# Optimization experiments

Measured on AMD Instinct MI355X. Metric: run time of the kernel, lower is better.

## Reference

```python
import jax, jax.numpy as jnp
import numpy as np

INPUT_SIZE = 16
K = 50
HIDDEN_COUNT = 25
FINAL_WIDTH = INPUT_SIZE + HIDDEN_COUNT * K  # 1266


def setup_inputs() -> dict:
    key = jax.random.key(0)
    k1, k2, k3, k4, k5 = jax.random.split(key, 5)
    B = 32768
    state = jax.random.normal(k1, (B, INPUT_SIZE), dtype=jnp.float32)
    # Zero-padded weight stack: layer i uses Ws[i, :, : INPUT_SIZE + i*K]
    Ws = jax.random.normal(k2, (HIDDEN_COUNT, K, FINAL_WIDTH), dtype=jnp.float32) * 0.05
    bs = jax.random.normal(k3, (HIDDEN_COUNT, K), dtype=jnp.float32) * 0.05
    Wout = jax.random.normal(k4, (FINAL_WIDTH, 1), dtype=jnp.float32) * 0.05
    bout = jax.random.normal(k5, (1,), dtype=jnp.float32) * 0.05
    return {"state": state, "Ws": Ws, "bs": bs, "Wout": Wout, "bout": bout}


def reference(state, Ws, bs, Wout, bout):
    x = state  # [B, 16], grows by 50 per layer
    for i in range(HIDDEN_COUNT):  # fixed-size structural loop over layers
        width = INPUT_SIZE + i * K
        w = Ws[i, :, :width]                       # [50, width] (static slice)
        y = jax.nn.leaky_relu(x @ w.T + bs[i], negative_slope=0.01)  # [B, 50]
        x = jnp.concatenate([x, y], axis=1)        # [B, width+50]
    return x @ Wout + bout  # [B, 1]
```

## Files before the change

kernel.cpp:

```cpp
#include <hip/hip_runtime.h>


#define IN 16
#define KJ 50
#define NL 25
#define FW 1266
#define TR 24
#define NB 1366
#define BTOT 32768
#define XSTR 1288
#define NTHREADS 512
#define XLO_OFF 61824
#define SLAB_OFF 123648
#define WOUT_OFF 148224
#define BIAS_OFF 153344
#define LDS_BYTES 158464
#define CHUNK_STRIDE 3200
#define TOTAL_CHUNKS 973

typedef __attribute__((ext_vector_type(8))) short bf16x8;
typedef __attribute__((ext_vector_type(16))) float f32x16;

__device__ __forceinline__ unsigned short bf16_hi(float x, float* hif) {
    unsigned u = __float_as_uint(x);
    unsigned h = (u + 0x8000u) >> 16;
    *hif = __uint_as_float(h << 16);
    return (unsigned short)h;
}
__device__ __forceinline__ unsigned short bf16_rnd(float x) {
    return (unsigned short)((__float_as_uint(x) + 0x8000u) >> 16);
}

__device__ __forceinline__ void split8(const float* __restrict__ rowp, int kb, int width,
                                       unsigned hi[4], unsigned lo[4]) {
#pragma unroll
    for (int p = 0; p < 4; ++p) {
        unsigned h2[2], l2[2];
#pragma unroll
        for (int q = 0; q < 2; ++q) {
            int k = kb + p * 2 + q;
            float v = (k < width) ? rowp[k] : 0.f;
            float hif;
            unsigned short h = bf16_hi(v, &hif);
            h2[q] = h;
            l2[q] = bf16_rnd(v - hif);
        }
        hi[p] = h2[0] | (h2[1] << 16);
        lo[p] = l2[0] | (l2[1] << 16);
    }
}

__global__ __launch_bounds__(64, 1) void split_w(const float* __restrict__ Ws,
                                                 char* __restrict__ wsbuf) {
    int rem = blockIdx.x, layer = 0;
    size_t off = 0;
    for (;;) {
        int c = (IN + KJ * layer + 15) >> 4;
        if (rem < c) break;
        rem -= c; off += (size_t)c * CHUNK_STRIDE; ++layer;
    }
    const int ci = rem, k0 = ci << 4, width = IN + KJ * layer;
    const float* Wl = Ws + (size_t)layer * KJ * FW;
    char* base = wsbuf + off + (size_t)ci * CHUNK_STRIDE;
    const int l = threadIdx.x, ll = l & 31, kh = l >> 5;
    const int kb = k0 + kh * 8;

    unsigned hi[4], lo[4];
    split8(Wl + (size_t)ll * FW, kb, width, hi, lo);
    *reinterpret_cast<uint4*>(base + l * 16)        = make_uint4(hi[0], hi[1], hi[2], hi[3]);
    *reinterpret_cast<uint4*>(base + 1024 + l * 16) = make_uint4(lo[0], lo[1], lo[2], lo[3]);
    if (ll < 18) {
        split8(Wl + (size_t)(32 + ll) * FW, kb, width, hi, lo);
        *reinterpret_cast<uint4*>(base + 2048 + (kh * 18 + ll) * 16) = make_uint4(hi[0], hi[1], hi[2], hi[3]);
        *reinterpret_cast<uint4*>(base + 2624 + (kh * 18 + ll) * 16) = make_uint4(lo[0], lo[1], lo[2], lo[3]);
    }
}

__device__ __forceinline__ void loadB2(const char* __restrict__ wb, int ci, int chunks,
                                       int n, int l, int ll, int kh,
                                       bf16x8& bh, bf16x8& bl) {
    bf16x8 z = {0, 0, 0, 0, 0, 0, 0, 0};
    bh = z; bl = z;
    if (ci < chunks) {
        const char* cb = wb + (size_t)ci * CHUNK_STRIDE;
        if (n == 0) {
            bh = *(const bf16x8*)(cb + l * 16);
            bl = *(const bf16x8*)(cb + 1024 + l * 16);
        } else if (ll < 18) {
            bh = *(const bf16x8*)(cb + (kh * 18 + ll) * 16);
            bl = *(const bf16x8*)(cb + 576 + (kh * 18 + ll) * 16);
        }
    }
}
__device__ __forceinline__ void loadG2(const char* __restrict__ wb, int c0, int chunks,
                                       int n, int l, int ll, int kh,
                                       bf16x8& b0h, bf16x8& b0l, bf16x8& b1h, bf16x8& b1l) {
    loadB2(wb, c0,     chunks, n, l, ll, kh, b0h, b0l);
    loadB2(wb, c0 + 4, chunks, n, l, ll, kh, b1h, b1l);
}

__device__ __forceinline__ void mfma3(const unsigned short* xrh, const unsigned short* xrl,
                                      int kof, const bf16x8 bh, const bf16x8 bl, f32x16& acc) {
    bf16x8 ah = *(const bf16x8*)(xrh + kof);
    bf16x8 al = *(const bf16x8*)(xrl + kof);
    acc = __builtin_amdgcn_mfma_f32_32x32x16_bf16(al, bh, acc, 0, 0, 0);
    acc = __builtin_amdgcn_mfma_f32_32x32x16_bf16(ah, bl, acc, 0, 0, 0);
    acc = __builtin_amdgcn_mfma_f32_32x32x16_bf16(ah, bh, acc, 0, 0, 0);
}

__global__ __launch_bounds__(NTHREADS, 2) void densenet_mfma(
    const float* __restrict__ state, const char* __restrict__ wsbuf,
    const float* __restrict__ bs,    const float* __restrict__ Wout,
    const float* __restrict__ bout,  float* __restrict__ out)
{
    __shared__ __align__(16) char lds[LDS_BYTES];
    unsigned short* xhi = (unsigned short*)lds;
    unsigned short* xlo = (unsigned short*)(lds + XLO_OFF);
    float* slab  = (float*)(lds + SLAB_OFF);
    float* woutl = (float*)(lds + WOUT_OFF);
    float* biasl = (float*)(lds + BIAS_OFF);

    const int tid = threadIdx.x;
    const int w   = tid >> 6;
    const int l   = tid & 63;
    const int ll  = l & 31, kh = l >> 5;
    const int kq  = w & 3;
    const int n   = w >> 2;
    const long row0 = (long)blockIdx.x * TR;

    {
        unsigned* p = (unsigned*)lds;
        for (int i = tid; i < (XLO_OFF * 2) / 4; i += NTHREADS) p[i] = 0u;
    }
    for (int i = tid; i < FW; i += NTHREADS)      woutl[i] = Wout[i];
    for (int i = tid; i < NL * KJ; i += NTHREADS) biasl[i] = bs[i];
    __syncthreads();
    if (tid < TR * IN) {
        int r = tid >> 4, c = tid & 15;
        if (row0 + r < BTOT) {
            float v = state[(row0 + r) * IN + c];
            float hif;
            xhi[r * XSTR + c] = bf16_hi(v, &hif);
            xlo[r * XSTR + c] = bf16_rnd(v - hif);
        }
    }
    __syncthreads();

    const unsigned short* xrh = xhi + ll * XSTR + (kh << 3);
    const unsigned short* xrl = xlo + ll * XSTR + (kh << 3);

    int width = IN;
    size_t wofs = 0;
    for (int layer = 0; layer < NL; ++layer) {
        const int chunks = (width + 15) >> 4;
        const char* wb = wsbuf + wofs + (n ? 2048 : 0);

        f32x16 a0, a1, a2, a3;
#pragma unroll
        for (int i = 0; i < 16; ++i) { a0[i] = 0.f; a1[i] = 0.f; a2[i] = 0.f; a3[i] = 0.f; }

        const int T  = (chunks > kq) ? ((chunks - kq + 3) >> 2) : 0;
        int NG = (T + 1) >> 1;
        NG += (NG & 1);

        if (NG > 0) {
            bf16x8 A0h, A0l, A1h, A1l, B0h, B0l, B1h, B1l;
            loadG2(wb, kq, chunks, n, l, ll, kh, A0h, A0l, A1h, A1l);
            for (int G = 0; G < NG; G += 2) {
                const int c0 = kq + (G << 3);
                loadG2(wb, c0 + 8, chunks, n, l, ll, kh, B0h, B0l, B1h, B1l);
                mfma3(xrh, xrl, (c0)     << 4, A0h, A0l, a0);
                mfma3(xrh, xrl, (c0 + 4) << 4, A1h, A1l, a1);
                if (G + 2 < NG)
                    loadG2(wb, c0 + 16, chunks, n, l, ll, kh, A0h, A0l, A1h, A1l);
                mfma3(xrh, xrl, (c0 + 8)  << 4, B0h, B0l, a2);
                mfma3(xrh, xrl, (c0 + 12) << 4, B1h, B1l, a3);
            }
        }

        {
            float* sl = slab + kq * 1536;
#pragma unroll
            for (int r = 0; r < 12; ++r) {
                float v = (a0[r] + a1[r]) + (a2[r] + a3[r]);
                int crow = (r & 3) + 8 * (r >> 2) + 4 * kh;
                sl[crow * 64 + n * 32 + ll] = v;
            }
        }
        __syncthreads();

#pragma unroll
        for (int it = 0; it < 3; ++it) {
            int idx = it * NTHREADS + tid;
            int row = idx >> 6, j = idx & 63;
            float s = (slab[row * 64 + j] + slab[1536 + row * 64 + j])
                    + (slab[3072 + row * 64 + j] + slab[4608 + row * 64 + j]);
            if (j < KJ) {
                s += biasl[layer * KJ + j];
                s = (s > 0.f) ? s : 0.01f * s;
                float hif;
                xhi[row * XSTR + width + j] = bf16_hi(s, &hif);
                xlo[row * XSTR + width + j] = bf16_rnd(s - hif);
            }
        }
        __syncthreads();

        width += KJ;
        wofs += (size_t)chunks * CHUNK_STRIDE;
    }

    const float b0 = bout[0];
#pragma unroll
    for (int rr = 0; rr < 3; ++rr) {
        const int row = w * 3 + rr;
        const long grow = row0 + row;
        const unsigned short* xh = xhi + row * XSTR;
        const unsigned short* xl = xlo + row * XSTR;
        float s = 0.f;
#pragma unroll
        for (int it = 0; it < 19; ++it) {
            int k = l + (it << 6);
            float xv = __uint_as_float((unsigned)xh[k] << 16)
                     + __uint_as_float((unsigned)xl[k] << 16);
            s += xv * woutl[k];
        }
        {
            int k = 1216 + l;
            if (k < FW) {
                float xv = __uint_as_float((unsigned)xh[k] << 16)
                         + __uint_as_float((unsigned)xl[k] << 16);
                s += xv * woutl[k];
            }
        }
#pragma unroll
        for (int m = 32; m >= 1; m >>= 1) s += __shfl_xor(s, m, 64);
        if (l == 0 && grow < BTOT) out[grow] = s + b0;
    }
}

extern "C" void kernel_launch(void* const* d_in, const int* in_sizes, int n_in,
                              void* d_out, int out_size, void* d_ws, size_t ws_size,
                              hipStream_t stream) {
    const float* state = (const float*)d_in[0];
    const float* Ws    = (const float*)d_in[1];
    const float* bs    = (const float*)d_in[2];
    const float* Wout  = (const float*)d_in[3];
    const float* bout  = (const float*)d_in[4];
    float* out = (float*)d_out;
    char* wsbuf = (char*)d_ws;

    split_w<<<dim3(TOTAL_CHUNKS), dim3(64), 0, stream>>>(Ws, wsbuf);
    densenet_mfma<<<dim3(NB), dim3(NTHREADS), 0, stream>>>(state, wsbuf, bs, Wout, bout, out);
}
```

Measured before the change: 512.3 us.

## Double block to 1024 threads with 8-way K split per output tile

Raises the workgroup from 8 to 16 waves, splitting the reduction (K) dimension of each layer 8 ways instead of 4. Each wave now keeps two accumulators instead of four. The cross-wave reduction is done in two passes through a smaller LDS slab to fit memory. Wout is read from global memory instead of being staged in LDS, and the X stride is shrunk to free space. The aim is more waves to hide MFMA and load latency, at the cost of an extra pair of barriers per layer and shorter per-wave K loops. The launch bound asks for 4 waves per SIMD, but with about 156 KB of LDS only one block can be resident per CU.

```diff
diff --git a/kernel.cpp b/kernel.cpp
--- a/kernel.cpp
+++ b/kernel.cpp
@@ -8,13 +8,12 @@
 #define TR 24
 #define NB 1366
 #define BTOT 32768
-#define XSTR 1288
-#define NTHREADS 512
-#define XLO_OFF 61824
-#define SLAB_OFF 123648
-#define WOUT_OFF 148224
-#define BIAS_OFF 153344
-#define LDS_BYTES 158464
+#define XSTR 1272
+#define NTHREADS 1024
+#define XLO_OFF 61056
+#define SLAB_OFF 122112
+#define BIAS_OFF 154880
+#define LDS_BYTES 159880
 #define CHUNK_STRIDE 3200
 #define TOTAL_CHUNKS 973
 
@@ -92,12 +91,6 @@
         }
     }
 }
-__device__ __forceinline__ void loadG2(const char* __restrict__ wb, int c0, int chunks,
-                                       int n, int l, int ll, int kh,
-                                       bf16x8& b0h, bf16x8& b0l, bf16x8& b1h, bf16x8& b1l) {
-    loadB2(wb, c0,     chunks, n, l, ll, kh, b0h, b0l);
-    loadB2(wb, c0 + 4, chunks, n, l, ll, kh, b1h, b1l);
-}
 
 __device__ __forceinline__ void mfma3(const unsigned short* xrh, const unsigned short* xrl,
                                       int kof, const bf16x8 bh, const bf16x8 bl, f32x16& acc) {
@@ -108,7 +101,7 @@
     acc = __builtin_amdgcn_mfma_f32_32x32x16_bf16(ah, bh, acc, 0, 0, 0);
 }
 
-__global__ __launch_bounds__(NTHREADS, 2) void densenet_mfma(
+__global__ __launch_bounds__(NTHREADS, 4) void densenet_mfma(
     const float* __restrict__ state, const char* __restrict__ wsbuf,
     const float* __restrict__ bs,    const float* __restrict__ Wout,
     const float* __restrict__ bout,  float* __restrict__ out)
@@ -117,22 +110,20 @@
     unsigned short* xhi = (unsigned short*)lds;
     unsigned short* xlo = (unsigned short*)(lds + XLO_OFF);
     float* slab  = (float*)(lds + SLAB_OFF);
-    float* woutl = (float*)(lds + WOUT_OFF);
     float* biasl = (float*)(lds + BIAS_OFF);
 
     const int tid = threadIdx.x;
     const int w   = tid >> 6;
     const int l   = tid & 63;
     const int ll  = l & 31, kh = l >> 5;
-    const int kq  = w & 3;
-    const int n   = w >> 2;
+    const int kq  = w & 7;
+    const int n   = w >> 3;
     const long row0 = (long)blockIdx.x * TR;
 
     {
         unsigned* p = (unsigned*)lds;
-        for (int i = tid; i < (XLO_OFF * 2) / 4; i += NTHREADS) p[i] = 0u;
-    }
-    for (int i = tid; i < FW; i += NTHREADS)      woutl[i] = Wout[i];
+        for (int i = tid; i < SLAB_OFF / 4; i += NTHREADS) p[i] = 0u;
+    }
     for (int i = tid; i < NL * KJ; i += NTHREADS) biasl[i] = bs[i];
     __syncthreads();
     if (tid < TR * IN) {
@@ -155,46 +146,40 @@
         const int chunks = (width + 15) >> 4;
         const char* wb = wsbuf + wofs + (n ? 2048 : 0);
 
-        f32x16 a0, a1, a2, a3;
-#pragma unroll
-        for (int i = 0; i < 16; ++i) { a0[i] = 0.f; a1[i] = 0.f; a2[i] = 0.f; a3[i] = 0.f; }
-
-        const int T  = (chunks > kq) ? ((chunks - kq + 3) >> 2) : 0;
-        int NG = (T + 1) >> 1;
-        NG += (NG & 1);
-
-        if (NG > 0) {
-            bf16x8 A0h, A0l, A1h, A1l, B0h, B0l, B1h, B1l;
-            loadG2(wb, kq, chunks, n, l, ll, kh, A0h, A0l, A1h, A1l);
-            for (int G = 0; G < NG; G += 2) {
-                const int c0 = kq + (G << 3);
-                loadG2(wb, c0 + 8, chunks, n, l, ll, kh, B0h, B0l, B1h, B1l);
-                mfma3(xrh, xrl, (c0)     << 4, A0h, A0l, a0);
-                mfma3(xrh, xrl, (c0 + 4) << 4, A1h, A1l, a1);
-                if (G + 2 < NG)
-                    loadG2(wb, c0 + 16, chunks, n, l, ll, kh, A0h, A0l, A1h, A1l);
-                mfma3(xrh, xrl, (c0 + 8)  << 4, B0h, B0l, a2);
-                mfma3(xrh, xrl, (c0 + 12) << 4, B1h, B1l, a3);
-            }
-        }
-
-        {
-            float* sl = slab + kq * 1536;
-#pragma unroll
-            for (int r = 0; r < 12; ++r) {
-                float v = (a0[r] + a1[r]) + (a2[r] + a3[r]);
+        f32x16 a0, a1;
+#pragma unroll
+        for (int i = 0; i < 16; ++i) { a0[i] = 0.f; a1[i] = 0.f; }
+
+        bf16x8 A0h, A0l, A1h, A1l, B0h, B0l, B1h, B1l;
+        loadB2(wb, kq,     chunks, n, l, ll, kh, A0h, A0l);
+        loadB2(wb, kq + 8, chunks, n, l, ll, kh, A1h, A1l);
+        for (int c0 = kq; c0 < chunks; c0 += 32) {
+            loadB2(wb, c0 + 16, chunks, n, l, ll, kh, B0h, B0l);
+            loadB2(wb, c0 + 24, chunks, n, l, ll, kh, B1h, B1l);
+            mfma3(xrh, xrl, c0 << 4, A0h, A0l, a0);
+            if (c0 + 8 < chunks)  mfma3(xrh, xrl, (c0 + 8) << 4, A1h, A1l, a1);
+            if (c0 + 32 < chunks) {
+                loadB2(wb, c0 + 32, chunks, n, l, ll, kh, A0h, A0l);
+                loadB2(wb, c0 + 40, chunks, n, l, ll, kh, A1h, A1l);
+            }
+            if (c0 + 16 < chunks) mfma3(xrh, xrl, (c0 + 16) << 4, B0h, B0l, a0);
+            if (c0 + 24 < chunks) mfma3(xrh, xrl, (c0 + 24) << 4, B1h, B1l, a1);
+        }
+
+        {
+            float* s1 = slab + kq * 1024 + n * 32 + ll;
+#pragma unroll
+            for (int r = 0; r < 8; ++r) {
                 int crow = (r & 3) + 8 * (r >> 2) + 4 * kh;
-                sl[crow * 64 + n * 32 + ll] = v;
-            }
-        }
-        __syncthreads();
-
-#pragma unroll
-        for (int it = 0; it < 3; ++it) {
-            int idx = it * NTHREADS + tid;
-            int row = idx >> 6, j = idx & 63;
-            float s = (slab[row * 64 + j] + slab[1536 + row * 64 + j])
-                    + (slab[3072 + row * 64 + j] + slab[4608 + row * 64 + j]);
+                s1[crow * 64] = a0[r] + a1[r];
+            }
+        }
+        __syncthreads();
+        {
+            int row = tid >> 6, j = tid & 63;
+            float s = 0.f;
+#pragma unroll
+            for (int q = 0; q < 8; ++q) s += slab[q * 1024 + row * 64 + j];
             if (j < KJ) {
                 s += biasl[layer * KJ + j];
                 s = (s > 0.f) ? s : 0.01f * s;
@@ -204,6 +189,30 @@
             }
         }
         __syncthreads();
+        {
+            float* s2 = slab + kq * 512 + n * 32 + ll;
+#pragma unroll
+            for (int r = 0; r < 4; ++r) {
+                int lrow = (r & 3) + 4 * kh;
+                s2[lrow * 64] = a0[8 + r] + a1[8 + r];
+            }
+        }
+        __syncthreads();
+        if (tid < 512) {
+            int lrow = tid >> 6, j = tid & 63;
+            int row = 16 + lrow;
+            float s = 0.f;
+#pragma unroll
+            for (int q = 0; q < 8; ++q) s += slab[q * 512 + lrow * 64 + j];
+            if (j < KJ) {
+                s += biasl[layer * KJ + j];
+                s = (s > 0.f) ? s : 0.01f * s;
+                float hif;
+                xhi[row * XSTR + width + j] = bf16_hi(s, &hif);
+                xlo[row * XSTR + width + j] = bf16_rnd(s - hif);
+            }
+        }
+        __syncthreads();
 
         width += KJ;
         wofs += (size_t)chunks * CHUNK_STRIDE;
@@ -211,8 +220,9 @@
 
     const float b0 = bout[0];
 #pragma unroll
-    for (int rr = 0; rr < 3; ++rr) {
-        const int row = w * 3 + rr;
+    for (int rr = 0; rr < 2; ++rr) {
+        if (rr == 1 && w >= 8) break;
+        const int row = rr ? 16 + w : w;
         const long grow = row0 + row;
         const unsigned short* xh = xhi + row * XSTR;
         const unsigned short* xl = xlo + row * XSTR;
@@ -222,14 +232,14 @@
             int k = l + (it << 6);
             float xv = __uint_as_float((unsigned)xh[k] << 16)
                      + __uint_as_float((unsigned)xl[k] << 16);
-            s += xv * woutl[k];
+            s += xv * Wout[k];
         }
         {
             int k = 1216 + l;
             if (k < FW) {
                 float xv = __uint_as_float((unsigned)xh[k] << 16)
                          + __uint_as_float((unsigned)xl[k] << 16);
-                s += xv * woutl[k];
+                s += xv * Wout[k];
             }
         }
 #pragma unroll
```

New measurement: 500.5 us. -2.3%, faster.
